# Optimization experiments

Measured on AMD Instinct MI355X. Metric: run time of the kernel, lower is better.

Reference implementation:

```python
import jax, jax.numpy as jnp
import numpy as np

N_NODES = 20000
IN_C = 512
OUT_C = 128
HEADS = 4
N_EDGES = 320000
NEG_SLOPE = 0.2


def setup_inputs() -> dict:
    key = jax.random.key(0)
    ks = jax.random.split(key, 10)
    x = jax.random.normal(ks[0], (N_NODES, IN_C), dtype=jnp.float32)
    edge_index = jax.random.randint(ks[1], (2, N_EDGES), 0, N_NODES, dtype=jnp.int64)
    s = 0.05
    return {
        "x": x,
        "edge_index": edge_index,
        "W1": jax.random.normal(ks[2], (IN_C, HEADS * OUT_C), dtype=jnp.float32) * s,
        "a_src1": jax.random.normal(ks[3], (HEADS, OUT_C), dtype=jnp.float32) * s,
        "a_dst1": jax.random.normal(ks[4], (HEADS, OUT_C), dtype=jnp.float32) * s,
        "b1": jnp.zeros((HEADS * OUT_C,), dtype=jnp.float32),
        "W2": jax.random.normal(ks[5], (HEADS * OUT_C, 1 * OUT_C), dtype=jnp.float32) * s,
        "a_src2": jax.random.normal(ks[6], (1, OUT_C), dtype=jnp.float32) * s,
        "a_dst2": jax.random.normal(ks[7], (1, OUT_C), dtype=jnp.float32) * s,
        "b2": jnp.zeros((OUT_C,), dtype=jnp.float32),
    }


def gat_conv(x, src, dst, W, a_src, a_dst, b, heads, out_c, concat):
    N = x.shape[0]
    h = (x @ W).reshape(N, heads, out_c)            # [N,H,C]
    al_src = jnp.sum(h * a_src, axis=-1)            # [N,H]
    al_dst = jnp.sum(h * a_dst, axis=-1)            # [N,H]
    e = jax.nn.leaky_relu(al_src[src] + al_dst[dst], NEG_SLOPE)  # [E,H]
    # segment softmax over edges grouped by destination node
    e_max = jax.ops.segment_max(e, dst, num_segments=N)         # [N,H]
    e = jnp.exp(e - e_max[dst])
    denom = jax.ops.segment_sum(e, dst, num_segments=N)         # [N,H]
    alpha = e / (denom[dst] + 1e-16)                             # [E,H]
    msg = h[src] * alpha[:, :, None]                             # [E,H,C]
    out = jax.ops.segment_sum(msg, dst, num_segments=N)          # [N,H,C]
    out = out.reshape(N, heads * out_c) if concat else jnp.mean(out, axis=1)
    return out + b


def reference(x, edge_index, W1, a_src1, a_dst1, b1, W2, a_src2, a_dst2, b2):
    N = x.shape[0]
    # PyG GATConv adds self-loops by default
    loops = jnp.arange(N, dtype=edge_index.dtype)
    src = jnp.concatenate([edge_index[0], loops])
    dst = jnp.concatenate([edge_index[1], loops])
    h = gat_conv(x, src, dst, W1, a_src1, a_dst1, b1, HEADS, OUT_C, concat=True)
    h = jax.nn.elu(h)
    return gat_conv(h, src, dst, W2, a_src2, a_dst2, b2, 1, OUT_C, concat=False)
```

## Files before the change

### kernel.cpp

```cpp
#include <hip/hip_runtime.h>
#include <hip/hip_bf16.h>

typedef __hip_bfloat16 bf16;
typedef __bf16 bf16x8 __attribute__((ext_vector_type(8)));
typedef float f32x4 __attribute__((ext_vector_type(4)));

#define NEG_SLOPE 0.2f
#define F32_THRESH 256


__device__ __forceinline__ bool is_f32(const int* fcnt) { return *fcnt > F32_THRESH; }

__device__ __forceinline__ float ld_f(const void* p, long long i, bool f32) {
    return f32 ? ((const float*)p)[i] : __bfloat162float(((const bf16*)p)[i]);
}

__device__ __forceinline__ float b2f(unsigned hs) {
    return __uint_as_float(hs << 16);
}

__device__ __forceinline__ unsigned pack_bf2(float a, float b) {
    union { bf16 h[2]; unsigned u; } p;
    p.h[0] = __float2bfloat16(a);
    p.h[1] = __float2bfloat16(b);
    return p.u;
}

__device__ __forceinline__ void load_lds16(const void* g, void* l) {
    __builtin_amdgcn_global_load_lds(
        (const __attribute__((address_space(1))) void*)g,
        (__attribute__((address_space(3))) void*)l, 16, 0, 0);
}


__global__ void k_probe(const unsigned* xw, long long nw, const int* idx, int n_half,
                        int* cnt, int* iflag) {
    long long t = blockIdx.x * (long long)blockDim.x + threadIdx.x;
    long long stride = (long long)gridDim.x * blockDim.x;
    int c = 0;
    for (long long i = t; i < nw; i += stride)
        if ((xw[i] & 0x7F80u) == 0x7F80u) c++;
    if (c) atomicAdd(cnt, c);
    int any = 0;
    for (long long i = t; i < n_half; i += stride)
        if (idx[2 * i + 1] != 0) any = 1;
    if (any) atomicOr(iflag, 1);
}


__global__ void k_tobf16(const void* src, const int* fcnt, bf16* dst,
                         long long n_valid, long long n_total) {
    if (!is_f32(fcnt)) return;
    long long t = blockIdx.x * (long long)blockDim.x + threadIdx.x;
    long long n8 = n_total / 8;
    for (long long i = t; i < n8; i += (long long)gridDim.x * blockDim.x) {
        long long b = i * 8;
        uint4 out;
        if (b + 8 <= n_valid) {
            const float4* s4 = (const float4*)src;
            float4 x0 = s4[i * 2], x1 = s4[i * 2 + 1];
            out.x = pack_bf2(x0.x, x0.y);
            out.y = pack_bf2(x0.z, x0.w);
            out.z = pack_bf2(x1.x, x1.y);
            out.w = pack_bf2(x1.z, x1.w);
        } else {
            bf16 tmp[8];
#pragma unroll
            for (int j = 0; j < 8; j++) {
                long long k = b + j;
                tmp[j] = (k < n_valid) ? __float2bfloat16(ld_f(src, k, true))
                                       : __float2bfloat16(0.f);
            }
            out = *(uint4*)tmp;
        }
        ((uint4*)dst)[i] = out;
    }
}

__global__ void k_tail(const void* x, const int* fcnt, bf16* tail, int R0, int Nrows, int K) {
    bool f32 = is_f32(fcnt);
    int total = 128 * K;
    for (int i = blockIdx.x * blockDim.x + threadIdx.x; i < total;
         i += gridDim.x * blockDim.x) {
        int r = i / K;
        long long src = (long long)(R0 + r) * K + (i - r * K);
        tail[i] = (R0 + r < Nrows) ? __float2bfloat16(ld_f(x, src, f32))
                                   : __float2bfloat16(0.f);
    }
}


__device__ __forceinline__ int edge_val(const void* idx, long long i, int is64) {
    return is64 ? (int)((const long long*)idx)[i] : ((const int*)idx)[i];
}

__global__ void k_count(const void* idx, const int* iflag, int E0, int N, int* deg) {
    int e = blockIdx.x * blockDim.x + threadIdx.x;
    if (e >= E0 + N) return;
    int is64 = (*iflag == 0);
    int d = (e < E0) ? edge_val(idx, (long long)E0 + e, is64) : (e - E0);
    if ((unsigned)d >= (unsigned)N) d = 0;
    atomicAdd(&deg[d], 1);
}

__global__ __launch_bounds__(1024) void k_scan(const int* deg, int* rowptr, int N) {
    __shared__ int part[1024];
    int t = threadIdx.x;
    int chunk = (N + 1023) / 1024;
    int s = t * chunk, e = min(N, s + chunk);
    int sum = 0;
    for (int i = s; i < e; i++) sum += deg[i];
    part[t] = sum;
    __syncthreads();
    for (int off = 1; off < 1024; off <<= 1) {
        int v = (t >= off) ? part[t - off] : 0;
        __syncthreads();
        part[t] += v;
        __syncthreads();
    }
    int run = (t == 0) ? 0 : part[t - 1];
    for (int i = s; i < e; i++) { rowptr[i] = run; run += deg[i]; }
    if (t == 1023) rowptr[N] = part[1023];
}

__global__ void k_scatter(const void* idx, const int* iflag, int E0, int N,
                          const int* rowptr, int* cursor, int* csr_src) {
    int e = blockIdx.x * blockDim.x + threadIdx.x;
    if (e >= E0 + N) return;
    int is64 = (*iflag == 0);
    int s, d;
    if (e < E0) {
        s = edge_val(idx, e, is64);
        d = edge_val(idx, (long long)E0 + e, is64);
    } else {
        s = d = e - E0;
    }
    if ((unsigned)s >= (unsigned)N) s = 0;
    if ((unsigned)d >= (unsigned)N) d = 0;
    int pos = rowptr[d] + atomicAdd(&cursor[d], 1);
    if ((unsigned)pos < (unsigned)(E0 + N)) csr_src[pos] = s;
}


__global__ void k_transpose(const void* W, const int* fcnt, bf16* Wt, int K, int N) {
    int i = blockIdx.x * blockDim.x + threadIdx.x;
    if (i >= K * N) return;
    bool f32 = is_f32(fcnt);
    int k = i / N, n = i % N;
    Wt[(size_t)n * K + k] = __float2bfloat16(ld_f(W, i, f32));
}


__global__ void k_al(const bf16* __restrict__ h, const void* a_s, const void* a_d,
                     const int* fcnt, float* als, float* ald, int N, int H) {
    __shared__ float sa[512], sd[512];
    const int HC = H * 128;
    bool f32 = is_f32(fcnt);
    for (int i = threadIdx.x; i < HC; i += blockDim.x) {
        sa[i] = ld_f(a_s, i, f32);
        sd[i] = ld_f(a_d, i, f32);
    }
    __syncthreads();
    int i = blockIdx.x * blockDim.x + threadIdx.x;
    if (i >= N * H) return;
    int n = i / H, hh = i % H;
    const uint4* row = (const uint4*)(h + (size_t)n * HC + hh * 128);
    float s = 0.f, d = 0.f;
#pragma unroll
    for (int q = 0; q < 16; q++) {
        uint4 u = row[q];
        unsigned uu[4] = {u.x, u.y, u.z, u.w};
#pragma unroll
        for (int t = 0; t < 4; t++) {
            float v0 = b2f(uu[t] & 0xFFFFu), v1 = b2f(uu[t] >> 16);
            int c = hh * 128 + q * 8 + t * 2;
            s += v0 * sa[c] + v1 * sa[c + 1];
            d += v0 * sd[c] + v1 * sd[c + 1];
        }
    }
    als[i] = s;
    ald[i] = d;
}


template <int BN, bool SEL>
__global__ __launch_bounds__(256) void k_gemm(const void* Araw, const bf16* Aconv,
                                              const bf16* Atail, const int* fcnt,
                                              const bf16* __restrict__ Bt,
                                              bf16* __restrict__ C,
                                              int M, int Nn, int K, int nfull) {
    constexpr int BM = 128, BK = 32;
    constexpr int NT = BN / 32;
    const int m0 = blockIdx.x * BM;
    const int n0 = blockIdx.y * BN;
    __shared__ __bf16 As[BM][BK];
    __shared__ __bf16 Bs[BN][BK];
    const int tid = threadIdx.x;
    const int wave = tid >> 6;
    const int lane = tid & 63;
    const int wm = (wave & 1) * 64;
    const int wn = (wave >> 1) * (NT * 16);
    const int lm = lane & 15;
    const int quad = lane >> 4;
    const int srow = tid >> 2;
    const int scol = (tid & 3) * 8;

    f32x4 acc[4][NT];
#pragma unroll
    for (int mt = 0; mt < 4; mt++)
#pragma unroll
        for (int nt = 0; nt < NT; nt++) acc[mt][nt] = (f32x4){0.f, 0.f, 0.f, 0.f};

    const bf16* Abase;
    int arow0;
    if (SEL) {
        const bf16* Asel = is_f32(fcnt) ? Aconv : (const bf16*)Araw;
        if ((int)blockIdx.x < nfull) { Abase = Asel; arow0 = m0; }
        else { Abase = Atail; arow0 = 0; }
    } else {
        Abase = (const bf16*)Araw;
        arow0 = m0;
    }

    const char* Ab = (const char*)(Abase + (size_t)(arow0 + srow) * K + scol);
    const char* Bb = (const char*)(Bt + (size_t)(n0 + srow) * K + scol);
    char* ldsA = (char*)&As[0][0] + wave * 1024;
    char* ldsB = (char*)&Bs[0][0] + wave * 1024;
    const size_t rstep = (size_t)64 * K * 2;

    for (int k0 = 0; k0 < K; k0 += BK) {
        __syncthreads();
        const size_t kb = (size_t)k0 * 2;
        load_lds16(Ab + kb, ldsA);
        load_lds16(Ab + kb + rstep, ldsA + 4096);
        load_lds16(Bb + kb, ldsB);
        if (BN == 128) load_lds16(Bb + kb + rstep, ldsB + 4096);
        __syncthreads();
        bf16x8 af[4], bfv[NT];
#pragma unroll
        for (int mt = 0; mt < 4; mt++)
            af[mt] = *(const bf16x8*)&As[wm + mt * 16 + lm][quad * 8];
#pragma unroll
        for (int nt = 0; nt < NT; nt++)
            bfv[nt] = *(const bf16x8*)&Bs[wn + nt * 16 + lm][quad * 8];
#pragma unroll
        for (int mt = 0; mt < 4; mt++)
#pragma unroll
            for (int nt = 0; nt < NT; nt++)
                acc[mt][nt] = __builtin_amdgcn_mfma_f32_16x16x32_bf16(
                    af[mt], bfv[nt], acc[mt][nt], 0, 0, 0);
    }

#pragma unroll
    for (int mt = 0; mt < 4; mt++) {
        int rb = m0 + wm + mt * 16 + quad * 4;
#pragma unroll
        for (int nt = 0; nt < NT; nt++) {
            int col = n0 + wn + nt * 16 + lm;
#pragma unroll
            for (int r = 0; r < 4; r++) {
                int row = rb + r;
                if (row < M) C[(size_t)row * Nn + col] = __float2bfloat16(acc[mt][nt][r]);
            }
        }
    }
}


template <int C, int H, bool ELU, bool DYN_OUT>
__global__ __launch_bounds__(256) void k_agg(
    const bf16* __restrict__ feat, const float* __restrict__ als,
    const float* __restrict__ ald, const int* __restrict__ rowptr,
    const int* __restrict__ csr_src, const void* bias, const int* fcnt,
    void* outp, int N, int E) {
    constexpr int CPL = C / 64;
    constexpr int Ch = C / H;
    const int wave = threadIdx.x >> 6;
    const int lane = threadIdx.x & 63;
    const int n = blockIdx.x * 4 + wave;
    if (n >= N) return;
    const int c0 = lane * CPL;
    const int head = c0 / Ch;

    int start = rowptr[n];
    if (start < 0) start = 0;
    int end = rowptr[n + 1];
    if (end > E) end = E;
    int deg = end - start;
    if (deg < 0) deg = 0;

    const float aldn = ald[(size_t)n * H + head];
    float acc[CPL] = {};
    float psum = 0.f;

    auto wfun = [&](int s) {
        float l = als[(size_t)s * H + head] + aldn;
        l = l > 0.f ? l : NEG_SLOPE * l;
        return __expf(fminf(l, 60.f));
    };
    auto body = [&](int s, float wl) {
        const bf16* fr = feat + (size_t)s * C + c0;
        if constexpr (CPL == 8) {
            uint4 u = *(const uint4*)fr;
            unsigned uu[4] = {u.x, u.y, u.z, u.w};
#pragma unroll
            for (int q = 0; q < 4; q++) {
                acc[2 * q] += wl * b2f(uu[q] & 0xFFFFu);
                acc[2 * q + 1] += wl * b2f(uu[q] >> 16);
            }
        } else {
            unsigned u = *(const unsigned*)fr;
            acc[0] += wl * b2f(u & 0xFFFFu);
            acc[1] += wl * b2f(u >> 16);
        }
    };

    int e = 0;
    for (; e + 4 <= deg; e += 4) {
        int i0 = start + e;
        int s0 = csr_src[i0], s1 = csr_src[i0 + 1];
        int s2 = csr_src[i0 + 2], s3 = csr_src[i0 + 3];
        if ((unsigned)s0 >= (unsigned)N) s0 = 0;
        if ((unsigned)s1 >= (unsigned)N) s1 = 0;
        if ((unsigned)s2 >= (unsigned)N) s2 = 0;
        if ((unsigned)s3 >= (unsigned)N) s3 = 0;
        float w0 = wfun(s0), w1 = wfun(s1), w2 = wfun(s2), w3 = wfun(s3);
        psum += w0 + w1 + w2 + w3;
        body(s0, w0);
        body(s1, w1);
        body(s2, w2);
        body(s3, w3);
    }
    for (; e < deg; e++) {
        int s = csr_src[start + e];
        if ((unsigned)s >= (unsigned)N) s = 0;
        float w0 = wfun(s);
        psum += w0;
        body(s, w0);
    }

    const float dn = psum + 1e-16f;
    const bool f32 = is_f32(fcnt);
#pragma unroll
    for (int j = 0; j < CPL; j++) {
        float v = acc[j] / dn + ld_f(bias, c0 + j, f32);
        if (ELU) v = v > 0.f ? v : expf(v) - 1.f;
        size_t oi = (size_t)n * C + c0 + j;
        if (DYN_OUT && f32) ((float*)outp)[oi] = v;
        else ((bf16*)outp)[oi] = __float2bfloat16(v);
    }
}


extern "C" void kernel_launch(void* const* d_in, const int* in_sizes, int n_in,
                              void* d_out, int out_size, void* d_ws, size_t ws_size,
                              hipStream_t stream) {
    const int N = in_sizes[0] / 512;
    const int K = 512;
    const int C1 = 512;
    const int C2 = 128;
    const int H1 = 4;
    const int E0 = in_sizes[1] / 2;
    const int E = E0 + N;
    const int Mpad = (N + 127) / 128 * 128;
    const int nfull = N / 128;

    const void* x_raw = d_in[0];
    const void* eidx = d_in[1];
    const void* W1 = d_in[2];
    const void* as1 = d_in[3];
    const void* ad1 = d_in[4];
    const void* b1 = d_in[5];
    const void* W2 = d_in[6];
    const void* as2 = d_in[7];
    const void* ad2 = d_in[8];
    const void* b2 = d_in[9];

    char* ws = (char*)d_ws;
    size_t off = 0;
    auto take = [&](size_t bytes) {
        size_t r = off;
        off += (bytes + 255) & ~(size_t)255;
        return r;
    };
    bf16* xb     = (bf16*)(ws + take((size_t)Mpad * K * 2));
    bf16* xtail  = (bf16*)(ws + take((size_t)128 * K * 2));
    bf16* h1     = (bf16*)(ws + take((size_t)N * C1 * 2));
    bf16* hagg   = (bf16*)(ws + take((size_t)Mpad * C1 * 2));
    bf16* W1t    = (bf16*)(ws + take((size_t)K * C1 * 2));
    bf16* W2t    = (bf16*)(ws + take((size_t)C1 * C2 * 2));
    float* al1s  = (float*)(ws + take((size_t)N * H1 * 4));
    float* al1d  = (float*)(ws + take((size_t)N * H1 * 4));
    int* rowptr  = (int*)(ws + take((size_t)(N + 1) * 4));
    int* csr_src = (int*)(ws + take((size_t)E * 4));
    int* deg     = (int*)(ws + take((size_t)(2 * N + 2) * 4));
    int* cursor  = deg + N;
    int* iflag   = deg + 2 * N;
    int* fcnt    = deg + 2 * N + 1;
    bf16* h2     = xb;
    float* al2s  = al1s;
    float* al2d  = al1d;
    if (off > ws_size) return;

    hipMemsetAsync(deg, 0, (size_t)(2 * N + 2) * 4, stream);
    hipMemsetAsync(hagg + (size_t)N * C1, 0, (size_t)(Mpad - N) * C1 * 2, stream);

    long long nw = (long long)in_sizes[0] / 2;
    if (nw > (1 << 20)) nw = 1 << 20;
    int nh = E0 > (1 << 16) ? (1 << 16) : E0;
    k_probe<<<256, 256, 0, stream>>>((const unsigned*)x_raw, nw, (const int*)eidx, nh,
                                     fcnt, iflag);

    k_count<<<(E + 255) / 256, 256, 0, stream>>>(eidx, iflag, E0, N, deg);
    k_scan<<<1, 1024, 0, stream>>>(deg, rowptr, N);
    k_scatter<<<(E + 255) / 256, 256, 0, stream>>>(eidx, iflag, E0, N, rowptr, cursor,
                                                   csr_src);

    k_tobf16<<<1024, 256, 0, stream>>>(x_raw, fcnt, xb, (long long)N * K,
                                       (long long)Mpad * K);
    k_tail<<<64, 256, 0, stream>>>(x_raw, fcnt, xtail, nfull * 128, N, K);
    k_transpose<<<(K * C1 + 255) / 256, 256, 0, stream>>>(W1, fcnt, W1t, K, C1);
    k_transpose<<<(C1 * C2 + 255) / 256, 256, 0, stream>>>(W2, fcnt, W2t, C1, C2);

    dim3 g1(Mpad / 128, C1 / 128);
    k_gemm<128, true><<<g1, 256, 0, stream>>>(x_raw, xb, xtail, fcnt, W1t, h1,
                                              N, C1, K, nfull);
    k_al<<<(N * H1 + 255) / 256, 256, 0, stream>>>(h1, as1, ad1, fcnt, al1s, al1d, N, H1);
    k_agg<512, 4, true, false><<<(N + 3) / 4, 256, 0, stream>>>(
        h1, al1s, al1d, rowptr, csr_src, b1, fcnt, hagg, N, E);

    dim3 g2(Mpad / 128, C2 / 64);
    k_gemm<64, false><<<g2, 256, 0, stream>>>(hagg, nullptr, nullptr, fcnt, W2t, h2,
                                              N, C2, C1, 0);
    k_al<<<(N + 255) / 256, 256, 0, stream>>>(h2, as2, ad2, fcnt, al2s, al2d, N, 1);
    k_agg<128, 1, false, true><<<(N + 3) / 4, 256, 0, stream>>>(
        h2, al2s, al2d, rowptr, csr_src, b2, fcnt, d_out, N, E);
}
```

Before: 326.7 us.

## Merge prep kernels into one launch and software-pipeline edge gathers in aggregation

Four preprocessing kernels (f32 to bf16 conversion, tail copy, two weight transposes) and a padding memset are folded into a single block-partitioned k_prep launch, cutting launch and inter-kernel gaps. The aggregation loop is rewritten as a double-buffered pipeline: the next batch's source indices and feature rows are loaded while the current batch is accumulated, with masked lanes padding partial batches. This raises register pressure and may hurt occupancy in k_agg.

```diff
diff --git a/kernel.cpp b/kernel.cpp
--- a/kernel.cpp
+++ b/kernel.cpp
@@ -31,6 +31,28 @@
         (const __attribute__((address_space(1))) void*)g,
         (__attribute__((address_space(3))) void*)l, 16, 0, 0);
 }
+
+template <int CPL> struct FV;
+template <> struct FV<8> {
+    uint4 v;
+    __device__ __forceinline__ void load(const bf16* p) { v = *(const uint4*)p; }
+    __device__ __forceinline__ void fma(float* acc, float w) const {
+        unsigned uu[4] = {v.x, v.y, v.z, v.w};
+#pragma unroll
+        for (int q = 0; q < 4; q++) {
+            acc[2 * q] += w * b2f(uu[q] & 0xFFFFu);
+            acc[2 * q + 1] += w * b2f(uu[q] >> 16);
+        }
+    }
+};
+template <> struct FV<2> {
+    unsigned v;
+    __device__ __forceinline__ void load(const bf16* p) { v = *(const unsigned*)p; }
+    __device__ __forceinline__ void fma(float* acc, float w) const {
+        acc[0] += w * b2f(v & 0xFFFFu);
+        acc[1] += w * b2f(v >> 16);
+    }
+};
 
 
 __global__ void k_probe(const unsigned* xw, long long nw, const int* idx, int n_half,
@@ -45,48 +67,6 @@
     for (long long i = t; i < n_half; i += stride)
         if (idx[2 * i + 1] != 0) any = 1;
     if (any) atomicOr(iflag, 1);
-}
-
-
-__global__ void k_tobf16(const void* src, const int* fcnt, bf16* dst,
-                         long long n_valid, long long n_total) {
-    if (!is_f32(fcnt)) return;
-    long long t = blockIdx.x * (long long)blockDim.x + threadIdx.x;
-    long long n8 = n_total / 8;
-    for (long long i = t; i < n8; i += (long long)gridDim.x * blockDim.x) {
-        long long b = i * 8;
-        uint4 out;
-        if (b + 8 <= n_valid) {
-            const float4* s4 = (const float4*)src;
-            float4 x0 = s4[i * 2], x1 = s4[i * 2 + 1];
-            out.x = pack_bf2(x0.x, x0.y);
-            out.y = pack_bf2(x0.z, x0.w);
-            out.z = pack_bf2(x1.x, x1.y);
-            out.w = pack_bf2(x1.z, x1.w);
-        } else {
-            bf16 tmp[8];
-#pragma unroll
-            for (int j = 0; j < 8; j++) {
-                long long k = b + j;
-                tmp[j] = (k < n_valid) ? __float2bfloat16(ld_f(src, k, true))
-                                       : __float2bfloat16(0.f);
-            }
-            out = *(uint4*)tmp;
-        }
-        ((uint4*)dst)[i] = out;
-    }
-}
-
-__global__ void k_tail(const void* x, const int* fcnt, bf16* tail, int R0, int Nrows, int K) {
-    bool f32 = is_f32(fcnt);
-    int total = 128 * K;
-    for (int i = blockIdx.x * blockDim.x + threadIdx.x; i < total;
-         i += gridDim.x * blockDim.x) {
-        int r = i / K;
-        long long src = (long long)(R0 + r) * K + (i - r * K);
-        tail[i] = (R0 + r < Nrows) ? __float2bfloat16(ld_f(x, src, f32))
-                                   : __float2bfloat16(0.f);
-    }
 }
 
 
@@ -142,12 +122,62 @@
 }
 
 
-__global__ void k_transpose(const void* W, const int* fcnt, bf16* Wt, int K, int N) {
-    int i = blockIdx.x * blockDim.x + threadIdx.x;
-    if (i >= K * N) return;
-    bool f32 = is_f32(fcnt);
-    int k = i / N, n = i % N;
-    Wt[(size_t)n * K + k] = __float2bfloat16(ld_f(W, i, f32));
+__global__ void k_prep(const void* x, const int* fcnt, bf16* xb, bf16* xtail,
+                       const void* W1, bf16* W1t, const void* W2, bf16* W2t,
+                       bf16* hpad, int hpad_elems, int N, int K, int C1, int C2,
+                       int R0, long long n_valid, long long n_total) {
+    const int b = blockIdx.x;
+    const int tid = threadIdx.x;
+    const bool f32 = is_f32(fcnt);
+    if (b < 512) {
+        if (!f32) return;
+        long long n8 = n_total / 8;
+        for (long long i = (long long)b * 256 + tid; i < n8; i += 512LL * 256) {
+            long long base = i * 8;
+            uint4 out;
+            if (base + 8 <= n_valid) {
+                const float4* s4 = (const float4*)x;
+                float4 x0 = s4[i * 2], x1 = s4[i * 2 + 1];
+                out.x = pack_bf2(x0.x, x0.y);
+                out.y = pack_bf2(x0.z, x0.w);
+                out.z = pack_bf2(x1.x, x1.y);
+                out.w = pack_bf2(x1.z, x1.w);
+            } else {
+                bf16 tmp[8];
+#pragma unroll
+                for (int j = 0; j < 8; j++) {
+                    long long k = base + j;
+                    tmp[j] = (k < n_valid) ? __float2bfloat16(ld_f(x, k, true))
+                                           : __float2bfloat16(0.f);
+                }
+                out = *(uint4*)tmp;
+            }
+            ((uint4*)xb)[i] = out;
+        }
+    } else if (b < 528) {
+        int total = 128 * K;
+        for (int i = (b - 512) * 256 + tid; i < total; i += 16 * 256) {
+            int r = i / K;
+            long long src = (long long)(R0 + r) * K + (i - r * K);
+            xtail[i] = (R0 + r < N) ? __float2bfloat16(ld_f(x, src, f32))
+                                    : __float2bfloat16(0.f);
+        }
+    } else if (b < 656) {
+        int total = K * C1;
+        for (int i = (b - 528) * 256 + tid; i < total; i += 128 * 256) {
+            int k = i / C1, n = i - k * C1;
+            W1t[(size_t)n * K + k] = __float2bfloat16(ld_f(W1, i, f32));
+        }
+    } else if (b < 688) {
+        int total = C1 * C2;
+        for (int i = (b - 656) * 256 + tid; i < total; i += 32 * 256) {
+            int k = i / C2, n = i - k * C2;
+            W2t[(size_t)n * C1 + k] = __float2bfloat16(ld_f(W2, i, f32));
+        }
+    } else {
+        for (int i = (b - 688) * 256 + tid; i < hpad_elems; i += 16 * 256)
+            hpad[i] = __float2bfloat16(0.f);
+    }
 }
 
 
@@ -293,50 +323,65 @@
     float acc[CPL] = {};
     float psum = 0.f;
 
-    auto wfun = [&](int s) {
-        float l = als[(size_t)s * H + head] + aldn;
-        l = l > 0.f ? l : NEG_SLOPE * l;
-        return __expf(fminf(l, 60.f));
-    };
-    auto body = [&](int s, float wl) {
-        const bf16* fr = feat + (size_t)s * C + c0;
-        if constexpr (CPL == 8) {
-            uint4 u = *(const uint4*)fr;
-            unsigned uu[4] = {u.x, u.y, u.z, u.w};
-#pragma unroll
-            for (int q = 0; q < 4; q++) {
-                acc[2 * q] += wl * b2f(uu[q] & 0xFFFFu);
-                acc[2 * q + 1] += wl * b2f(uu[q] >> 16);
-            }
-        } else {
-            unsigned u = *(const unsigned*)fr;
-            acc[0] += wl * b2f(u & 0xFFFFu);
-            acc[1] += wl * b2f(u >> 16);
-        }
-    };
-
-    int e = 0;
-    for (; e + 4 <= deg; e += 4) {
-        int i0 = start + e;
-        int s0 = csr_src[i0], s1 = csr_src[i0 + 1];
-        int s2 = csr_src[i0 + 2], s3 = csr_src[i0 + 3];
-        if ((unsigned)s0 >= (unsigned)N) s0 = 0;
-        if ((unsigned)s1 >= (unsigned)N) s1 = 0;
-        if ((unsigned)s2 >= (unsigned)N) s2 = 0;
-        if ((unsigned)s3 >= (unsigned)N) s3 = 0;
-        float w0 = wfun(s0), w1 = wfun(s1), w2 = wfun(s2), w3 = wfun(s3);
-        psum += w0 + w1 + w2 + w3;
-        body(s0, w0);
-        body(s1, w1);
-        body(s2, w2);
-        body(s3, w3);
-    }
-    for (; e < deg; e++) {
-        int s = csr_src[start + e];
-        if ((unsigned)s >= (unsigned)N) s = 0;
-        float w0 = wfun(s);
-        psum += w0;
-        body(s, w0);
+    if (deg > 0) {
+        const int nb = (deg + 3) >> 2;
+
+        auto load_idx = [&](int b, int* s, float* m) {
+#pragma unroll
+            for (int j = 0; j < 4; j++) {
+                int e = b * 4 + j;
+                bool v = e < deg;
+                int sv = csr_src[start + (v ? e : 0)];
+                if ((unsigned)sv >= (unsigned)N) sv = 0;
+                s[j] = sv;
+                m[j] = v ? 1.f : 0.f;
+            }
+        };
+        auto load_data = [&](const int* s, float* a, FV<CPL>* f) {
+#pragma unroll
+            for (int j = 0; j < 4; j++) {
+                a[j] = als[(size_t)s[j] * H + head];
+                f[j].load(feat + (size_t)s[j] * C + c0);
+            }
+        };
+
+        int sP[4];
+        float mP[4];
+        float aC[4], mC[4];
+        FV<CPL> fC[4];
+
+        load_idx(0, sP, mP);
+        load_data(sP, aC, fC);
+#pragma unroll
+        for (int j = 0; j < 4; j++) mC[j] = mP[j];
+        if (nb > 1) load_idx(1, sP, mP);
+
+        for (int b = 0;; b++) {
+            float aN[4], mN[4];
+            FV<CPL> fN[4];
+            bool more = (b + 1) < nb;
+            if (more) {
+                load_data(sP, aN, fN);
+#pragma unroll
+                for (int j = 0; j < 4; j++) mN[j] = mP[j];
+                if (b + 2 < nb) load_idx(b + 2, sP, mP);
+            }
+#pragma unroll
+            for (int j = 0; j < 4; j++) {
+                float l = aC[j] + aldn;
+                l = l > 0.f ? l : NEG_SLOPE * l;
+                float w = mC[j] * __expf(fminf(l, 60.f));
+                psum += w;
+                fC[j].fma(acc, w);
+            }
+            if (!more) break;
+#pragma unroll
+            for (int j = 0; j < 4; j++) {
+                aC[j] = aN[j];
+                mC[j] = mN[j];
+                fC[j] = fN[j];
+            }
+        }
     }
 
     const float dn = psum + 1e-16f;
@@ -403,7 +448,6 @@
     if (off > ws_size) return;
 
     hipMemsetAsync(deg, 0, (size_t)(2 * N + 2) * 4, stream);
-    hipMemsetAsync(hagg + (size_t)N * C1, 0, (size_t)(Mpad - N) * C1 * 2, stream);
 
     long long nw = (long long)in_sizes[0] / 2;
     if (nw > (1 << 20)) nw = 1 << 20;
@@ -416,11 +460,10 @@
     k_scatter<<<(E + 255) / 256, 256, 0, stream>>>(eidx, iflag, E0, N, rowptr, cursor,
                                                    csr_src);
 
-    k_tobf16<<<1024, 256, 0, stream>>>(x_raw, fcnt, xb, (long long)N * K,
-                                       (long long)Mpad * K);
-    k_tail<<<64, 256, 0, stream>>>(x_raw, fcnt, xtail, nfull * 128, N, K);
-    k_transpose<<<(K * C1 + 255) / 256, 256, 0, stream>>>(W1, fcnt, W1t, K, C1);
-    k_transpose<<<(C1 * C2 + 255) / 256, 256, 0, stream>>>(W2, fcnt, W2t, C1, C2);
+    k_prep<<<704, 256, 0, stream>>>(x_raw, fcnt, xb, xtail, W1, W1t, W2, W2t,
+                                    hagg + (size_t)N * C1, (Mpad - N) * C1,
+                                    N, K, C1, C2, nfull * 128,
+                                    (long long)N * K, (long long)Mpad * K);
 
     dim3 g1(Mpad / 128, C1 / 128);
     k_gemm<128, true><<<g1, 256, 0, stream>>>(x_raw, xb, xtail, fcnt, W1t, h1,
```

Measured after the change: 317.4 us. -2.8%, faster.
